# Kernel tuning notes

Hardware: AMD Instinct MI355X
Metric: run time of the kernel (lower is better)

Reference implementation:

```python
import jax, jax.numpy as jnp
import numpy as np

N = 8192
HID = 64
TAU = 0.8
LAMBDA = 0.5
POS_DENSITY = 0.005


def setup_inputs() -> dict:
    key = jax.random.key(0)
    k1, k2, k3, k4, k5, k6, k7 = jax.random.split(key, 7)
    x1 = jax.random.normal(k1, (N, HID), dtype=jnp.float32)
    x2 = jax.random.normal(k2, (N, HID), dtype=jnp.float32)
    # xavier_uniform with gain=1.414 for square [HID, HID] linears
    limit = 1.414 * np.sqrt(6.0 / (HID + HID))
    W1 = jax.random.uniform(k3, (HID, HID), dtype=jnp.float32, minval=-limit, maxval=limit)
    b1 = jnp.zeros((HID,), dtype=jnp.float32)
    W2 = jax.random.uniform(k4, (HID, HID), dtype=jnp.float32, minval=-limit, maxval=limit)
    b2 = jnp.zeros((HID,), dtype=jnp.float32)
    pm = (jax.random.uniform(k5, (N, N), dtype=jnp.float32) < POS_DENSITY).astype(jnp.float32)
    positive_matrix = jnp.maximum(pm, jnp.eye(N, dtype=jnp.float32))
    return {"x1": x1, "x2": x2, "W1": W1, "b1": b1, "W2": W2, "b2": b2,
            "positive_matrix": positive_matrix}


def _project(x, W1, b1, W2, b2):
    # nn.Linear(hidden, hidden) -> ELU -> nn.Linear(hidden, hidden)
    h = jax.nn.elu(x @ W1.T + b1)
    return h @ W2.T + b2


def _l2norm(z, eps=1e-12):
    # F.normalize(p=2, dim=1): x / max(||x||, eps)
    n = jnp.linalg.norm(z, axis=-1, keepdims=True)
    return z / jnp.maximum(n, eps)


def _sim(z1, z2, tau):
    return jnp.exp((_l2norm(z1) @ _l2norm(z2).T) / tau)  # [N, N]


def _masked_loss(sim_mat, pos):
    row = sim_mat / (jnp.sum(sim_mat, axis=-1, keepdims=True) + 1e-8)
    return -jnp.log(jnp.sum(row * pos, axis=-1) + 1e-8).mean()


def reference(x1, x2, W1, b1, W2, b2, positive_matrix):
    z1 = _project(x1, W1, b1, W2, b2)
    z2 = _project(x2, W1, b1, W2, b2)
    sc_mp = _sim(z1, z2, TAU)
    mp_sc = _sim(z2, z1, TAU)
    sc_loss = _masked_loss(sc_mp, positive_matrix)
    mp_loss = _masked_loss(mp_sc, positive_matrix)
    return sc_loss * LAMBDA + mp_loss * (1.0 - LAMBDA)
```

## Files before the change

### kernel.cpp

```cpp
#include <hip/hip_runtime.h>
#include <hip/hip_bf16.h>

#define N 8192
#define HID 64
#define JC 16

typedef __attribute__((ext_vector_type(4))) float f32x4;
typedef __attribute__((ext_vector_type(8))) __bf16 bf16x8;

__global__ __launch_bounds__(256) void proj_kernel(
    const float* __restrict__ x1, const float* __restrict__ x2,
    const float* __restrict__ W1, const float* __restrict__ b1,
    const float* __restrict__ W2, const float* __restrict__ b2,
    __bf16* __restrict__ Z1h, __bf16* __restrict__ Z2h)
{
  __shared__ __align__(16) float w1s[64*68];
  __shared__ __align__(16) float w2s[64*68];
  __shared__ __align__(16) float xs[4][64];
  __shared__ __align__(16) float hs[4][64];

  const int tid  = threadIdx.x;
  const int lane = tid & 63;
  const int w    = tid >> 6;

  for (int idx = tid; idx < 64*64; idx += 256) {
    int j = idx >> 6, k = idx & 63;
    w1s[j*68+k] = W1[idx];
    w2s[j*68+k] = W2[idx];
  }
  __syncthreads();

  const float bias1 = b1[lane];
  const float bias2 = b2[lane];

  const int wave_global = blockIdx.x * 4 + w;
  #pragma unroll 1
  for (int it = 0; it < 4; ++it) {
    int R = wave_global * 4 + it;
    const float* src; __bf16* dst;
    if (R < N) { src = x1 + (size_t)R*HID;      dst = Z1h + (size_t)R*HID; }
    else       { src = x2 + (size_t)(R-N)*HID;  dst = Z2h + (size_t)(R-N)*HID; }

    float xv = src[lane];
    xs[w][lane] = xv;
    float acc = bias1;
    #pragma unroll
    for (int qq = 0; qq < 16; ++qq) {
      f32x4 xq = *(const f32x4*)&xs[w][qq*4];
      f32x4 wq = *(const f32x4*)&w1s[lane*68 + qq*4];
      acc += xq.x*wq.x + xq.y*wq.y + xq.z*wq.z + xq.w*wq.w;
    }
    float h = acc > 0.f ? acc : expm1f(acc);
    hs[w][lane] = h;
    float acc2 = bias2;
    #pragma unroll
    for (int qq = 0; qq < 16; ++qq) {
      f32x4 hq = *(const f32x4*)&hs[w][qq*4];
      f32x4 wq = *(const f32x4*)&w2s[lane*68 + qq*4];
      acc2 += hq.x*wq.x + hq.y*wq.y + hq.z*wq.z + hq.w*wq.w;
    }
    float z = acc2;
    float ss = z*z;
    #pragma unroll
    for (int m = 1; m < 64; m <<= 1) ss += __shfl_xor(ss, m);
    float inv = 1.0f / fmaxf(sqrtf(ss), 1e-12f);
    dst[lane] = (__bf16)(z * inv);
  }
}

__global__ __launch_bounds__(256, 6) void sim_kernel(
    const __bf16* __restrict__ Z1h, const __bf16* __restrict__ Z2h,
    const float* __restrict__ pos,
    float* __restrict__ rowsum1, float* __restrict__ num1,
    float* __restrict__ rowsum2, float* __restrict__ num2)
{
  const int tid  = threadIdx.x;
  const int lane = tid & 63;
  const int w    = tid >> 6;
  const int r16  = lane & 15;
  const int q    = lane >> 4;

  const int bi = blockIdx.x / JC;
  const int jc = blockIdx.x % JC;
  const int i0 = bi*64 + w*16;

  const __bf16* z1r = Z1h + (size_t)(i0 + r16)*HID + q*8;
  const __bf16* z2r = Z2h + (size_t)(i0 + r16)*HID + q*8;
  bf16x8 a1lo = *(const bf16x8*)(z1r);
  bf16x8 a1hi = *(const bf16x8*)(z1r + 32);
  bf16x8 a2lo = *(const bf16x8*)(z2r);
  bf16x8 a2hi = *(const bf16x8*)(z2r + 32);

  float s1[4] = {0.f,0.f,0.f,0.f}, n1[4] = {0.f,0.f,0.f,0.f};
  float s2[4] = {0.f,0.f,0.f,0.f}, n2[4] = {0.f,0.f,0.f,0.f};

  const int jbeg = jc * (N/JC);
  const int jend = jbeg + (N/JC);
  const float Cexp = 1.8033688011112042f;

  const float* pbase = pos + (size_t)(i0 + q*4)*N + r16;

  #pragma unroll 1
  for (int j0 = jbeg; j0 < jend; j0 += 32) {
    bf16x8 b2l[2], b2h[2], b1l[2], b1h[2];
    float pv[2][4];
    #pragma unroll
    for (int c = 0; c < 2; ++c) {
      const __bf16* zb2 = Z2h + (size_t)(j0 + c*16 + r16)*HID + q*8;
      const __bf16* zb1 = Z1h + (size_t)(j0 + c*16 + r16)*HID + q*8;
      b2l[c] = *(const bf16x8*)(zb2);
      b2h[c] = *(const bf16x8*)(zb2 + 32);
      b1l[c] = *(const bf16x8*)(zb1);
      b1h[c] = *(const bf16x8*)(zb1 + 32);
      const float* pp = pbase + j0 + c*16;
      pv[c][0] = pp[0];
      pv[c][1] = pp[(size_t)N];
      pv[c][2] = pp[(size_t)2*N];
      pv[c][3] = pp[(size_t)3*N];
    }
    #pragma unroll
    for (int c = 0; c < 2; ++c) {
      f32x4 zero4 = {0.f,0.f,0.f,0.f};
      f32x4 d1 = __builtin_amdgcn_mfma_f32_16x16x32_bf16(a1lo, b2l[c], zero4, 0,0,0);
      d1       = __builtin_amdgcn_mfma_f32_16x16x32_bf16(a1hi, b2h[c], d1,    0,0,0);
      f32x4 d2 = __builtin_amdgcn_mfma_f32_16x16x32_bf16(a2lo, b1l[c], zero4, 0,0,0);
      d2       = __builtin_amdgcn_mfma_f32_16x16x32_bf16(a2hi, b1h[c], d2,    0,0,0);
      #pragma unroll
      for (int r = 0; r < 4; ++r) {
        float e1 = exp2f(d1[r] * Cexp);
        float e2 = exp2f(d2[r] * Cexp);
        s1[r] += e1; n1[r] += e1 * pv[c][r];
        s2[r] += e2; n2[r] += e2 * pv[c][r];
      }
    }
  }

  #pragma unroll
  for (int r = 0; r < 4; ++r) {
    #pragma unroll
    for (int m = 1; m < 16; m <<= 1) {
      s1[r] += __shfl_xor(s1[r], m);
      n1[r] += __shfl_xor(n1[r], m);
      s2[r] += __shfl_xor(s2[r], m);
      n2[r] += __shfl_xor(n2[r], m);
    }
  }
  if (r16 == 0) {
    #pragma unroll
    for (int r = 0; r < 4; ++r) {
      int row = i0 + q*4 + r;
      atomicAdd(&rowsum1[row], s1[r]);
      atomicAdd(&num1[row],    n1[r]);
      atomicAdd(&rowsum2[row], s2[r]);
      atomicAdd(&num2[row],    n2[r]);
    }
  }
}

__global__ __launch_bounds__(1024) void loss_kernel(
    const float* __restrict__ rowsum1, const float* __restrict__ num1,
    const float* __restrict__ rowsum2, const float* __restrict__ num2,
    float* __restrict__ out)
{
  __shared__ float part[16];
  const int tid = threadIdx.x, lane = tid & 63, w = tid >> 6;
  float acc = 0.f;
  for (int i = tid; i < N; i += 1024) {
    float sc = -logf(num1[i]/(rowsum1[i]+1e-8f) + 1e-8f);
    float mp = -logf(num2[i]/(rowsum2[i]+1e-8f) + 1e-8f);
    acc += 0.5f*sc + 0.5f*mp;
  }
  #pragma unroll
  for (int m = 1; m < 64; m <<= 1) acc += __shfl_xor(acc, m);
  if (lane == 0) part[w] = acc;
  __syncthreads();
  if (tid == 0) {
    float t = 0.f;
    #pragma unroll
    for (int k = 0; k < 16; ++k) t += part[k];
    out[0] = t * (1.0f/N);
  }
}

extern "C" void kernel_launch(void* const* d_in, const int* in_sizes, int n_in,
                              void* d_out, int out_size, void* d_ws, size_t ws_size,
                              hipStream_t stream) {
  const float* x1  = (const float*)d_in[0];
  const float* x2  = (const float*)d_in[1];
  const float* W1  = (const float*)d_in[2];
  const float* b1  = (const float*)d_in[3];
  const float* W2  = (const float*)d_in[4];
  const float* b2  = (const float*)d_in[5];
  const float* pos = (const float*)d_in[6];

  char* ws = (char*)d_ws;
  __bf16* Z1h = (__bf16*)ws;
  __bf16* Z2h = (__bf16*)(ws + (size_t)N*HID*sizeof(__bf16));
  size_t zbytes = (size_t)2*N*HID*sizeof(__bf16);
  float* rowsum1 = (float*)(ws + zbytes);
  float* num1    = rowsum1 + N;
  float* rowsum2 = num1 + N;
  float* num2    = rowsum2 + N;

  hipMemsetAsync(ws + zbytes, 0, (size_t)4*N*sizeof(float), stream);
  proj_kernel<<<1024, 256, 0, stream>>>(x1, x2, W1, b1, W2, b2, Z1h, Z2h);
  sim_kernel<<<128*JC, 256, 0, stream>>>(Z1h, Z2h, pos, rowsum1, num1, rowsum2, num2);
  loss_kernel<<<1, 1024, 0, stream>>>(rowsum1, num1, rowsum2, num2, (float*)d_out);
}
```

Measured before the change: 448.6 us.

## Double-buffer sim loads and transpose MFMA so positive mask loads vectorize

The sim kernel now keeps two register buffers and loads the next 32-column chunk while the current one is being computed, so global-load latency overlaps with MFMA and exp work. The MFMA operands are swapped so each lane's four outputs belong to one row and four adjacent columns. That lets the positive-mask reads become a single float4 load, and each lane needs one scalar accumulator per quantity. The final reduction shrinks to two shuffles per quantity. Occupancy is traded for the extra buffer registers by lowering the launch-bounds minimum from 6 to 4 blocks.

```diff
diff --git a/kernel.cpp b/kernel.cpp
--- a/kernel.cpp
+++ b/kernel.cpp
@@ -68,7 +68,7 @@
   }
 }
 
-__global__ __launch_bounds__(256, 6) void sim_kernel(
+__global__ __launch_bounds__(256, 4) void sim_kernel(
     const __bf16* __restrict__ Z1h, const __bf16* __restrict__ Z2h,
     const float* __restrict__ pos,
     float* __restrict__ rowsum1, float* __restrict__ num1,
@@ -86,74 +86,76 @@
 
   const __bf16* z1r = Z1h + (size_t)(i0 + r16)*HID + q*8;
   const __bf16* z2r = Z2h + (size_t)(i0 + r16)*HID + q*8;
-  bf16x8 a1lo = *(const bf16x8*)(z1r);
-  bf16x8 a1hi = *(const bf16x8*)(z1r + 32);
-  bf16x8 a2lo = *(const bf16x8*)(z2r);
-  bf16x8 a2hi = *(const bf16x8*)(z2r + 32);
-
-  float s1[4] = {0.f,0.f,0.f,0.f}, n1[4] = {0.f,0.f,0.f,0.f};
-  float s2[4] = {0.f,0.f,0.f,0.f}, n2[4] = {0.f,0.f,0.f,0.f};
+  const bf16x8 a1lo = *(const bf16x8*)(z1r);
+  const bf16x8 a1hi = *(const bf16x8*)(z1r + 32);
+  const bf16x8 a2lo = *(const bf16x8*)(z2r);
+  const bf16x8 a2hi = *(const bf16x8*)(z2r + 32);
+
+  float s1 = 0.f, n1 = 0.f, s2 = 0.f, n2 = 0.f;
 
   const int jbeg = jc * (N/JC);
-  const int jend = jbeg + (N/JC);
   const float Cexp = 1.8033688011112042f;
-
-  const float* pbase = pos + (size_t)(i0 + q*4)*N + r16;
-
+  const float* prow = pos + (size_t)(i0 + r16)*N + q*4;
+
+  bf16x8 Ab2l[2], Ab2h[2], Ab1l[2], Ab1h[2];
+  bf16x8 Bb2l[2], Bb2h[2], Bb1l[2], Bb1h[2];
+  f32x4  Apv[2],  Bpv[2];
+
+#define LOADJ(P, J) { \
+    _Pragma("unroll") \
+    for (int c = 0; c < 2; ++c) { \
+      const __bf16* zj2 = Z2h + (size_t)((J) + c*16 + r16)*HID + q*8; \
+      const __bf16* zj1 = Z1h + (size_t)((J) + c*16 + r16)*HID + q*8; \
+      P##b2l[c] = *(const bf16x8*)(zj2); \
+      P##b2h[c] = *(const bf16x8*)(zj2 + 32); \
+      P##b1l[c] = *(const bf16x8*)(zj1); \
+      P##b1h[c] = *(const bf16x8*)(zj1 + 32); \
+      P##pv[c]  = *(const f32x4*)(prow + (J) + c*16); \
+    } }
+
+#define COMPJ(P) { \
+    _Pragma("unroll") \
+    for (int c = 0; c < 2; ++c) { \
+      f32x4 zero4 = {0.f,0.f,0.f,0.f}; \
+      f32x4 d1 = __builtin_amdgcn_mfma_f32_16x16x32_bf16(P##b2l[c], a1lo, zero4, 0,0,0); \
+      d1       = __builtin_amdgcn_mfma_f32_16x16x32_bf16(P##b2h[c], a1hi, d1,    0,0,0); \
+      f32x4 d2 = __builtin_amdgcn_mfma_f32_16x16x32_bf16(P##b1l[c], a2lo, zero4, 0,0,0); \
+      d2       = __builtin_amdgcn_mfma_f32_16x16x32_bf16(P##b1h[c], a2hi, d2,    0,0,0); \
+      _Pragma("unroll") \
+      for (int r = 0; r < 4; ++r) { \
+        float e1 = exp2f(d1[r] * Cexp); \
+        float e2 = exp2f(d2[r] * Cexp); \
+        s1 += e1; n1 += e1 * P##pv[c][r]; \
+        s2 += e2; n2 += e2 * P##pv[c][r]; \
+      } \
+    } }
+
+  LOADJ(A, jbeg)
+  LOADJ(B, jbeg + 32)
   #pragma unroll 1
-  for (int j0 = jbeg; j0 < jend; j0 += 32) {
-    bf16x8 b2l[2], b2h[2], b1l[2], b1h[2];
-    float pv[2][4];
-    #pragma unroll
-    for (int c = 0; c < 2; ++c) {
-      const __bf16* zb2 = Z2h + (size_t)(j0 + c*16 + r16)*HID + q*8;
-      const __bf16* zb1 = Z1h + (size_t)(j0 + c*16 + r16)*HID + q*8;
-      b2l[c] = *(const bf16x8*)(zb2);
-      b2h[c] = *(const bf16x8*)(zb2 + 32);
-      b1l[c] = *(const bf16x8*)(zb1);
-      b1h[c] = *(const bf16x8*)(zb1 + 32);
-      const float* pp = pbase + j0 + c*16;
-      pv[c][0] = pp[0];
-      pv[c][1] = pp[(size_t)N];
-      pv[c][2] = pp[(size_t)2*N];
-      pv[c][3] = pp[(size_t)3*N];
-    }
-    #pragma unroll
-    for (int c = 0; c < 2; ++c) {
-      f32x4 zero4 = {0.f,0.f,0.f,0.f};
-      f32x4 d1 = __builtin_amdgcn_mfma_f32_16x16x32_bf16(a1lo, b2l[c], zero4, 0,0,0);
-      d1       = __builtin_amdgcn_mfma_f32_16x16x32_bf16(a1hi, b2h[c], d1,    0,0,0);
-      f32x4 d2 = __builtin_amdgcn_mfma_f32_16x16x32_bf16(a2lo, b1l[c], zero4, 0,0,0);
-      d2       = __builtin_amdgcn_mfma_f32_16x16x32_bf16(a2hi, b1h[c], d2,    0,0,0);
-      #pragma unroll
-      for (int r = 0; r < 4; ++r) {
-        float e1 = exp2f(d1[r] * Cexp);
-        float e2 = exp2f(d2[r] * Cexp);
-        s1[r] += e1; n1[r] += e1 * pv[c][r];
-        s2[r] += e2; n2[r] += e2 * pv[c][r];
-      }
-    }
-  }
-
-  #pragma unroll
-  for (int r = 0; r < 4; ++r) {
-    #pragma unroll
-    for (int m = 1; m < 16; m <<= 1) {
-      s1[r] += __shfl_xor(s1[r], m);
-      n1[r] += __shfl_xor(n1[r], m);
-      s2[r] += __shfl_xor(s2[r], m);
-      n2[r] += __shfl_xor(n2[r], m);
-    }
-  }
-  if (r16 == 0) {
-    #pragma unroll
-    for (int r = 0; r < 4; ++r) {
-      int row = i0 + q*4 + r;
-      atomicAdd(&rowsum1[row], s1[r]);
-      atomicAdd(&num1[row],    n1[r]);
-      atomicAdd(&rowsum2[row], s2[r]);
-      atomicAdd(&num2[row],    n2[r]);
-    }
+  for (int t = 0; t < 14; t += 2) {
+    COMPJ(A)
+    LOADJ(A, jbeg + (t+2)*32)
+    COMPJ(B)
+    LOADJ(B, jbeg + (t+3)*32)
+  }
+  COMPJ(A)
+  COMPJ(B)
+
+#undef LOADJ
+#undef COMPJ
+
+  s1 += __shfl_xor(s1, 16); s1 += __shfl_xor(s1, 32);
+  n1 += __shfl_xor(n1, 16); n1 += __shfl_xor(n1, 32);
+  s2 += __shfl_xor(s2, 16); s2 += __shfl_xor(s2, 32);
+  n2 += __shfl_xor(n2, 16); n2 += __shfl_xor(n2, 32);
+
+  if (lane < 16) {
+    int row = i0 + r16;
+    atomicAdd(&rowsum1[row], s1);
+    atomicAdd(&num1[row],    n1);
+    atomicAdd(&rowsum2[row], s2);
+    atomicAdd(&num2[row],    n2);
   }
 }
 
```

New measurement: 476.1 us. 6.1% more time.

## Split positive-mask numerator into sparse scan kernel, separate row-sum MFMA kernel

Applied to the files above, without the earlier changes.

Replaces the fused similarity kernel with two kernels. A scan kernel streams each row of the positive mask coalesced, finds nonzeros with ballot, and recomputes only those dot products for the numerator. A separate MFMA kernel computes the dense row sums without touching the mask. The 256 MB mask is still read once, but now with contiguous row loads instead of strided per-tile reads, and the dense kernel is lighter. In exchange there is an extra launch and serialized per-positive wave reductions; numerator dot products now use bf16 values accumulated in fp32 via shuffles.

```diff
diff --git a/kernel.cpp b/kernel.cpp
--- a/kernel.cpp
+++ b/kernel.cpp
@@ -68,11 +68,57 @@
   }
 }
 
-__global__ __launch_bounds__(256, 6) void sim_kernel(
+__global__ __launch_bounds__(256) void scan_kernel(
+    const float* __restrict__ pos,
     const __bf16* __restrict__ Z1h, const __bf16* __restrict__ Z2h,
-    const float* __restrict__ pos,
-    float* __restrict__ rowsum1, float* __restrict__ num1,
-    float* __restrict__ rowsum2, float* __restrict__ num2)
+    float* __restrict__ num1, float* __restrict__ num2)
+{
+  const int tid  = threadIdx.x;
+  const int lane = tid & 63;
+  const int w    = tid >> 6;
+  const int row  = blockIdx.x * 4 + w;
+  if (row >= N) return;
+
+  const float z1i = (float)Z1h[(size_t)row*HID + lane];
+  const float z2i = (float)Z2h[(size_t)row*HID + lane];
+  const float Cexp = 1.8033688011112042f;
+  const float* prow = pos + (size_t)row * N;
+
+  float n1 = 0.f, n2 = 0.f;
+
+  f32x4 v = *(const f32x4*)(prow + lane*4);
+  #pragma unroll 1
+  for (int it = 0; it < N/256; ++it) {
+    int itn = (it < N/256 - 1) ? (it + 1) : it;
+    f32x4 vn = *(const f32x4*)(prow + itn*256 + lane*4);
+    #pragma unroll
+    for (int s = 0; s < 4; ++s) {
+      unsigned long long m = __ballot(v[s] != 0.0f);
+      while (m) {
+        int l = __ffsll(m) - 1;
+        m &= m - 1;
+        int j = it*256 + l*4 + s;
+        float z1j = (float)Z1h[(size_t)j*HID + lane];
+        float z2j = (float)Z2h[(size_t)j*HID + lane];
+        float d1 = z1i * z2j;
+        float d2 = z2i * z1j;
+        #pragma unroll
+        for (int mm = 1; mm < 64; mm <<= 1) {
+          d1 += __shfl_xor(d1, mm);
+          d2 += __shfl_xor(d2, mm);
+        }
+        n1 += exp2f(d1 * Cexp);
+        n2 += exp2f(d2 * Cexp);
+      }
+    }
+    v = vn;
+  }
+  if (lane == 0) { num1[row] = n1; num2[row] = n2; }
+}
+
+__global__ __launch_bounds__(256) void sums_kernel(
+    const __bf16* __restrict__ Z1h, const __bf16* __restrict__ Z2h,
+    float* __restrict__ rowsum1, float* __restrict__ rowsum2)
 {
   const int tid  = threadIdx.x;
   const int lane = tid & 63;
@@ -86,24 +132,21 @@
 
   const __bf16* z1r = Z1h + (size_t)(i0 + r16)*HID + q*8;
   const __bf16* z2r = Z2h + (size_t)(i0 + r16)*HID + q*8;
-  bf16x8 a1lo = *(const bf16x8*)(z1r);
-  bf16x8 a1hi = *(const bf16x8*)(z1r + 32);
-  bf16x8 a2lo = *(const bf16x8*)(z2r);
-  bf16x8 a2hi = *(const bf16x8*)(z2r + 32);
-
-  float s1[4] = {0.f,0.f,0.f,0.f}, n1[4] = {0.f,0.f,0.f,0.f};
-  float s2[4] = {0.f,0.f,0.f,0.f}, n2[4] = {0.f,0.f,0.f,0.f};
+  const bf16x8 a1lo = *(const bf16x8*)(z1r);
+  const bf16x8 a1hi = *(const bf16x8*)(z1r + 32);
+  const bf16x8 a2lo = *(const bf16x8*)(z2r);
+  const bf16x8 a2hi = *(const bf16x8*)(z2r + 32);
+
+  float s1[4] = {0.f,0.f,0.f,0.f};
+  float s2[4] = {0.f,0.f,0.f,0.f};
 
   const int jbeg = jc * (N/JC);
   const int jend = jbeg + (N/JC);
   const float Cexp = 1.8033688011112042f;
 
-  const float* pbase = pos + (size_t)(i0 + q*4)*N + r16;
-
   #pragma unroll 1
   for (int j0 = jbeg; j0 < jend; j0 += 32) {
     bf16x8 b2l[2], b2h[2], b1l[2], b1h[2];
-    float pv[2][4];
     #pragma unroll
     for (int c = 0; c < 2; ++c) {
       const __bf16* zb2 = Z2h + (size_t)(j0 + c*16 + r16)*HID + q*8;
@@ -112,11 +155,6 @@
       b2h[c] = *(const bf16x8*)(zb2 + 32);
       b1l[c] = *(const bf16x8*)(zb1);
       b1h[c] = *(const bf16x8*)(zb1 + 32);
-      const float* pp = pbase + j0 + c*16;
-      pv[c][0] = pp[0];
-      pv[c][1] = pp[(size_t)N];
-      pv[c][2] = pp[(size_t)2*N];
-      pv[c][3] = pp[(size_t)3*N];
     }
     #pragma unroll
     for (int c = 0; c < 2; ++c) {
@@ -127,10 +165,8 @@
       d2       = __builtin_amdgcn_mfma_f32_16x16x32_bf16(a2hi, b1h[c], d2,    0,0,0);
       #pragma unroll
       for (int r = 0; r < 4; ++r) {
-        float e1 = exp2f(d1[r] * Cexp);
-        float e2 = exp2f(d2[r] * Cexp);
-        s1[r] += e1; n1[r] += e1 * pv[c][r];
-        s2[r] += e2; n2[r] += e2 * pv[c][r];
+        s1[r] += exp2f(d1[r] * Cexp);
+        s2[r] += exp2f(d2[r] * Cexp);
       }
     }
   }
@@ -140,19 +176,15 @@
     #pragma unroll
     for (int m = 1; m < 16; m <<= 1) {
       s1[r] += __shfl_xor(s1[r], m);
-      n1[r] += __shfl_xor(n1[r], m);
       s2[r] += __shfl_xor(s2[r], m);
-      n2[r] += __shfl_xor(n2[r], m);
     }
   }
   if (r16 == 0) {
     #pragma unroll
     for (int r = 0; r < 4; ++r) {
-      int row = i0 + q*4 + r;
-      atomicAdd(&rowsum1[row], s1[r]);
-      atomicAdd(&num1[row],    n1[r]);
-      atomicAdd(&rowsum2[row], s2[r]);
-      atomicAdd(&num2[row],    n2[r]);
+      int rowi = i0 + q*4 + r;
+      atomicAdd(&rowsum1[rowi], s1[r]);
+      atomicAdd(&rowsum2[rowi], s2[r]);
     }
   }
 }
@@ -204,6 +236,7 @@
 
   hipMemsetAsync(ws + zbytes, 0, (size_t)4*N*sizeof(float), stream);
   proj_kernel<<<1024, 256, 0, stream>>>(x1, x2, W1, b1, W2, b2, Z1h, Z2h);
-  sim_kernel<<<128*JC, 256, 0, stream>>>(Z1h, Z2h, pos, rowsum1, num1, rowsum2, num2);
+  scan_kernel<<<2048, 256, 0, stream>>>(pos, Z1h, Z2h, num1, num2);
+  sums_kernel<<<128*JC, 256, 0, stream>>>(Z1h, Z2h, rowsum1, rowsum2);
   loss_kernel<<<1, 1024, 0, stream>>>(rowsum1, num1, rowsum2, num2, (float*)d_out);
 }
```

Measured after the change: 527.6 us. 17.6% more time.
